# Kernel tuning notes

Hardware: AMD Instinct MI355X
Metric: run time of the kernel (lower is better)

Reference implementation:

```python
import jax, jax.numpy as jnp
import numpy as np

N, C, K, D = 65536, 64, 16, 2
EPS = 1e-5


def batch_norm(x, g, b):
    # training-mode BatchNorm1d over rows (biased variance), x: [rows, C]
    m = x.mean(axis=0)
    v = ((x - m) ** 2).mean(axis=0)
    return (x - m) * jax.lax.rsqrt(v + EPS) * g + b


def setup_inputs() -> dict:
    key = jax.random.key(0)
    ks = jax.random.split(key, 20)
    s = 1.0 / np.sqrt(C)
    inp = {
        "coord": jax.random.normal(ks[0], (N, 3), jnp.float32),
        "feat": jax.random.normal(ks[1], (N, C), jnp.float32),
        "reference_index": jax.random.randint(ks[2], (N, K), 0, N, jnp.int32),
        # per-block stacked params, leading dim D
        "fc1_w": jax.random.uniform(ks[3], (D, C, C), jnp.float32, -s, s),
        "bn1_g": jnp.ones((D, C), jnp.float32),
        "bn1_b": jnp.zeros((D, C), jnp.float32),
        "la_w1": jax.random.uniform(ks[4], (D, C, C), jnp.float32, -s, s),
        "la_b1": jax.random.uniform(ks[5], (D, C), jnp.float32, -s, s),
        "la_bn1_g": jnp.ones((D, C), jnp.float32),
        "la_bn1_b": jnp.zeros((D, C), jnp.float32),
        "la_w2": jax.random.uniform(ks[6], (D, C, C), jnp.float32, -s, s),
        "la_b2": jax.random.uniform(ks[7], (D, C), jnp.float32, -s, s),
        "la_bn2_g": jnp.ones((D, C), jnp.float32),
        "la_bn2_b": jnp.zeros((D, C), jnp.float32),
        "fc3_w": jax.random.uniform(ks[8], (D, C, C), jnp.float32, -s, s),
        "bn2_g": jnp.ones((D, C), jnp.float32),
        "bn2_b": jnp.zeros((D, C), jnp.float32),
        "bn3_g": jnp.ones((D, C), jnp.float32),
        "bn3_b": jnp.zeros((D, C), jnp.float32),
    }
    return inp


def reference(coord, feat, reference_index,
              fc1_w, bn1_g, bn1_b,
              la_w1, la_b1, la_bn1_g, la_bn1_b,
              la_w2, la_b2, la_bn2_g, la_bn2_b,
              fc3_w, bn2_g, bn2_b, bn3_g, bn3_b):
    ref = reference_index  # [n, k]
    for d in range(D):
        identity = feat
        # fc1 (no bias) -> bn1 -> relu
        x = jax.nn.relu(batch_norm(feat @ fc1_w[d].T, bn1_g[d], bn1_b[d]))
        # LocalAggregation: gather neighbors, shared MLP on [n*k, c], max over k
        grouped = x[ref].reshape(-1, C)                      # [n*k, c]
        h = jax.nn.relu(batch_norm(grouped @ la_w1[d].T + la_b1[d],
                                   la_bn1_g[d], la_bn1_b[d]))
        h = jax.nn.relu(batch_norm(h @ la_w2[d].T + la_b2[d],
                                   la_bn2_g[d], la_bn2_b[d]))
        x = h.reshape(ref.shape[0], K, C).max(axis=1)        # [n, c]
        # bn2 -> relu -> fc3 (no bias) -> bn3
        x = jax.nn.relu(batch_norm(x, bn2_g[d], bn2_b[d]))
        x = batch_norm(x @ fc3_w[d].T, bn3_g[d], bn3_b[d])
        feat = jax.nn.relu(identity + x)
    return feat
```

## Files before the change

kernel.cpp:

```cpp
#include <hip/hip_runtime.h>

#define N_PTS 65536
#define BN_EPS 1e-5f
#define NSHD 16
#define NSB  (10 * NSHD * 128)

typedef __attribute__((ext_vector_type(8))) short bf16x8;
typedef __attribute__((ext_vector_type(4))) float f32x4;

static __device__ __forceinline__ unsigned short f2bf(float f) {
    unsigned u = __builtin_bit_cast(unsigned, f);
    u += 0x7fffu + ((u >> 16) & 1u);
    return (unsigned short)(u >> 16);
}
static __device__ __forceinline__ float bf2f(unsigned short h) {
    unsigned u = ((unsigned)h) << 16;
    return __builtin_bit_cast(float, u);
}
static __device__ __forceinline__ unsigned pack2(float a, float b) {
    return (unsigned)f2bf(a) | ((unsigned)f2bf(b) << 16);
}

template<int PRE, int BIAS, int WTD, int OUTBF, int INBF, int HIST>
__global__ __launch_bounds__(256, 4) void mm_kernel(
    const void*  __restrict__ inv_,  const float* __restrict__ identity,
    const float* __restrict__ Wg,    const float* __restrict__ bias,
    const float* __restrict__ gg,    const float* __restrict__ bb,
    const float* __restrict__ S_in,  float inv_denom,
    void*        __restrict__ outv,  float* __restrict__ S_out,
    const unsigned* __restrict__ cw, float* __restrict__ f1_out,
    const int* __restrict__ ref,     unsigned* __restrict__ hdst)
{
    __shared__ unsigned short lwh[64][72], lwl[64][72];
    __shared__ float stg[4][16][68];
    __shared__ float sc[64], sh[64];
    __shared__ float LS[4][64], LQ[4][64];

    const int tid  = threadIdx.x;
    const int lane = tid & 63, wid = tid >> 6;
    const int l15  = lane & 15, kg = lane >> 4;
    const int brow = blockIdx.x * 64;
    const int arow = brow + wid * 16 + l15;

    const int wr = tid >> 2, wc = (tid & 3) * 16;
    const float4* wp = (const float4*)(Wg + wr * 64 + wc);
    float4 wv0 = wp[0], wv1 = wp[1], wv2 = wp[2], wv3 = wp[3];

    float xv[2][8];
    uint4 ub0, ub1;
    float4 a0, a1, a2, a3;
    if (INBF) {
        const uint4* ap = (const uint4*)((const unsigned*)inv_ +
                                         (size_t)arow * 32 + kg * 4);
        ub0 = ap[0]; ub1 = ap[4];
    } else {
        const float4* ap = (const float4*)((const float*)inv_ +
                                           (size_t)arow * 64 + kg * 8);
        a0 = ap[0]; a1 = ap[1]; a2 = ap[8]; a3 = ap[9];
    }
    float4 i0, i1, i2, i3;
    if (PRE == 2) {
        const float4* ip = (const float4*)(identity + (size_t)arow * 64 + kg * 8);
        i0 = ip[0]; i1 = ip[1]; i2 = ip[8]; i3 = ip[9];
    }
    uint4 cc;
    if (WTD) cc = ((const uint4*)(cw + brow + wid * 16))[kg];
    if (HIST) {
        int4 hv = ((const int4*)(ref + brow * 16))[tid];
        atomicAdd(&hdst[hv.x], 1u); atomicAdd(&hdst[hv.y], 1u);
        atomicAdd(&hdst[hv.z], 1u); atomicAdd(&hdst[hv.w], 1u);
    }

    {
        float wf[16] = {wv0.x,wv0.y,wv0.z,wv0.w, wv1.x,wv1.y,wv1.z,wv1.w,
                        wv2.x,wv2.y,wv2.z,wv2.w, wv3.x,wv3.y,wv3.z,wv3.w};
        unsigned ph[8], pl[8];
        #pragma unroll
        for (int q = 0; q < 8; ++q) {
            unsigned short h0 = f2bf(wf[2*q]),   h1 = f2bf(wf[2*q+1]);
            unsigned short l0 = f2bf(wf[2*q]   - bf2f(h0));
            unsigned short l1 = f2bf(wf[2*q+1] - bf2f(h1));
            ph[q] = (unsigned)h0 | ((unsigned)h1 << 16);
            pl[q] = (unsigned)l0 | ((unsigned)l1 << 16);
        }
        uint4* dh = (uint4*)(&lwh[wr][wc]);
        uint4* dl = (uint4*)(&lwl[wr][wc]);
        dh[0] = make_uint4(ph[0], ph[1], ph[2], ph[3]);
        dh[1] = make_uint4(ph[4], ph[5], ph[6], ph[7]);
        dl[0] = make_uint4(pl[0], pl[1], pl[2], pl[3]);
        dl[1] = make_uint4(pl[4], pl[5], pl[6], pl[7]);
    }

    if (PRE >= 1) {
        if (tid < 64) {
            float s = 0.f, q = 0.f;
            #pragma unroll
            for (int g = 0; g < NSHD; ++g) {
                s += S_in[g * 128 + tid];
                q += S_in[g * 128 + 64 + tid];
            }
            float m   = s * inv_denom;
            float var = q * inv_denom - m * m;
            float scl = gg[tid] * rsqrtf(var + BN_EPS);
            sc[tid] = scl; sh[tid] = bb[tid] - m * scl;
        }
    }
    __syncthreads();

    if (INBF) {
        uint4 uu[2] = {ub0, ub1};
        #pragma unroll
        for (int ks = 0; ks < 2; ++ks) {
            unsigned w0 = uu[ks].x, w1 = uu[ks].y, w2 = uu[ks].z, w3 = uu[ks].w;
            xv[ks][0] = bf2f((unsigned short)(w0 & 0xffffu));
            xv[ks][1] = bf2f((unsigned short)(w0 >> 16));
            xv[ks][2] = bf2f((unsigned short)(w1 & 0xffffu));
            xv[ks][3] = bf2f((unsigned short)(w1 >> 16));
            xv[ks][4] = bf2f((unsigned short)(w2 & 0xffffu));
            xv[ks][5] = bf2f((unsigned short)(w2 >> 16));
            xv[ks][6] = bf2f((unsigned short)(w3 & 0xffffu));
            xv[ks][7] = bf2f((unsigned short)(w3 >> 16));
        }
    } else {
        xv[0][0]=a0.x; xv[0][1]=a0.y; xv[0][2]=a0.z; xv[0][3]=a0.w;
        xv[0][4]=a1.x; xv[0][5]=a1.y; xv[0][6]=a1.z; xv[0][7]=a1.w;
        xv[1][0]=a2.x; xv[1][1]=a2.y; xv[1][2]=a2.z; xv[1][3]=a2.w;
        xv[1][4]=a3.x; xv[1][5]=a3.y; xv[1][6]=a3.z; xv[1][7]=a3.w;
    }

    if (PRE == 1) {
        #pragma unroll
        for (int ks = 0; ks < 2; ++ks)
            #pragma unroll
            for (int j = 0; j < 8; ++j) {
                int k = ks * 32 + kg * 8 + j;
                xv[ks][j] = fmaxf(xv[ks][j] * sc[k] + sh[k], 0.f);
            }
    } else if (PRE == 2) {
        float idv[2][8];
        idv[0][0]=i0.x; idv[0][1]=i0.y; idv[0][2]=i0.z; idv[0][3]=i0.w;
        idv[0][4]=i1.x; idv[0][5]=i1.y; idv[0][6]=i1.z; idv[0][7]=i1.w;
        idv[1][0]=i2.x; idv[1][1]=i2.y; idv[1][2]=i2.z; idv[1][3]=i2.w;
        idv[1][4]=i3.x; idv[1][5]=i3.y; idv[1][6]=i3.z; idv[1][7]=i3.w;
        #pragma unroll
        for (int ks = 0; ks < 2; ++ks) {
            #pragma unroll
            for (int j = 0; j < 8; ++j) {
                int k = ks * 32 + kg * 8 + j;
                xv[ks][j] = fmaxf(idv[ks][j] + xv[ks][j] * sc[k] + sh[k], 0.f);
            }
            float* f1p = f1_out + (size_t)arow * 64 + kg * 8 + ks * 32;
            *(float4*)(f1p)     = make_float4(xv[ks][0], xv[ks][1], xv[ks][2], xv[ks][3]);
            *(float4*)(f1p + 4) = make_float4(xv[ks][4], xv[ks][5], xv[ks][6], xv[ks][7]);
        }
    }

    bf16x8 ahi[2], alo[2];
    #pragma unroll
    for (int ks = 0; ks < 2; ++ks) {
        bf16x8 th, tl;
        #pragma unroll
        for (int j = 0; j < 8; ++j) {
            unsigned short h = f2bf(xv[ks][j]);
            th[j] = (short)h;
            tl[j] = (short)f2bf(xv[ks][j] - bf2f(h));
        }
        ahi[ks] = th; alo[ks] = tl;
    }
    f32x4 d[4];
    #pragma unroll
    for (int ct = 0; ct < 4; ++ct) {
        float bc = BIAS ? bias[ct * 16 + l15] : 0.f;
        d[ct] = (f32x4){bc, bc, bc, bc};
    }
    #pragma unroll
    for (int ct = 0; ct < 4; ++ct) {
        const int gcol = ct * 16 + l15;
        #pragma unroll
        for (int ks = 0; ks < 2; ++ks) {
            bf16x8 wh = *(const bf16x8*)(&lwh[gcol][ks * 32 + kg * 8]);
            bf16x8 wl = *(const bf16x8*)(&lwl[gcol][ks * 32 + kg * 8]);
            d[ct] = __builtin_amdgcn_mfma_f32_16x16x32_bf16(ahi[ks], wh, d[ct], 0, 0, 0);
            d[ct] = __builtin_amdgcn_mfma_f32_16x16x32_bf16(alo[ks], wh, d[ct], 0, 0, 0);
            d[ct] = __builtin_amdgcn_mfma_f32_16x16x32_bf16(ahi[ks], wl, d[ct], 0, 0, 0);
        }
    }

    float wt[4] = {1.f, 1.f, 1.f, 1.f};
    if (WTD) {
        wt[0] = (float)cc.x; wt[1] = (float)cc.y;
        wt[2] = (float)cc.z; wt[3] = (float)cc.w;
    }
    float ts[4], tq[4];
    #pragma unroll
    for (int ct = 0; ct < 4; ++ct) {
        float t = 0.f, t2 = 0.f;
        #pragma unroll
        for (int i = 0; i < 4; ++i) {
            float v = d[ct][i];
            t += wt[i] * v; t2 += wt[i] * v * v;
        }
        ts[ct] = t; tq[ct] = t2;
    }

    #pragma unroll
    for (int ct = 0; ct < 4; ++ct)
        #pragma unroll
        for (int i = 0; i < 4; ++i)
            stg[wid][kg * 4 + i][ct * 16 + l15] = d[ct][i];
    __syncthreads();
    if (!OUTBF) {
        float* op = (float*)outv + (size_t)arow * 64 + kg * 16;
        const float* srow = &stg[wid][l15][kg * 16];
        *(float4*)(op + 0)  = *(const float4*)(srow + 0);
        *(float4*)(op + 4)  = *(const float4*)(srow + 4);
        *(float4*)(op + 8)  = *(const float4*)(srow + 8);
        *(float4*)(op + 12) = *(const float4*)(srow + 12);
    } else {
        const float* srow = &stg[wid][l15][kg * 16];
        unsigned pk[8];
        #pragma unroll
        for (int q = 0; q < 8; ++q) pk[q] = pack2(srow[2 * q], srow[2 * q + 1]);
        unsigned* op = (unsigned*)outv;
        uint4* dst = (uint4*)(op + (size_t)arow * 32 + kg * 8);
        dst[0] = make_uint4(pk[0], pk[1], pk[2], pk[3]);
        dst[1] = make_uint4(pk[4], pk[5], pk[6], pk[7]);
    }

    #pragma unroll
    for (int ct = 0; ct < 4; ++ct) {
        float a = ts[ct], b = tq[ct];
        a += __shfl_xor(a, 16);  a += __shfl_xor(a, 32);
        b += __shfl_xor(b, 16);  b += __shfl_xor(b, 32);
        if (kg == 0) { LS[wid][ct * 16 + l15] = a; LQ[wid][ct * 16 + l15] = b; }
    }
    __syncthreads();
    const int bsel = blockIdx.x & (NSHD - 1);
    if (tid < 64)
        atomicAdd(S_out + bsel * 128 + tid,
                  LS[0][tid] + LS[1][tid] + LS[2][tid] + LS[3][tid]);
    else if (tid < 128) {
        int c = tid - 64;
        atomicAdd(S_out + bsel * 128 + 64 + c,
                  LQ[0][c] + LQ[1][c] + LQ[2][c] + LQ[3][c]);
    }
}

__global__ __launch_bounds__(256) void gather_kernel(
    const unsigned* __restrict__ y3u, const int* __restrict__ ref,
    const float* __restrict__ S_in, float inv_denom,
    const float* __restrict__ gg, const float* __restrict__ bb,
    unsigned* __restrict__ xmu, float* __restrict__ S_out)
{
    __shared__ float scs[64], shs[64], Rs[256], Rq[256];
    const int tid = threadIdx.x;
    const int lane = tid & 63, wid = tid >> 6;
    const int c2 = lane & 31;
    const int hsel = lane & 32;
    const int p = blockIdx.x * 4 + wid;
    const int r = 2 * p + (hsel ? 1 : 0);

    int jv = ref[r * 16 + (lane & 15)];
    unsigned u[16];
    #pragma unroll
    for (int t = 0; t < 16; ++t) {
        int j = __shfl(jv, hsel + t);
        u[t] = y3u[(size_t)j * 32 + c2];
    }

    if (tid < 64) {
        float s = 0.f, q = 0.f;
        #pragma unroll
        for (int g = 0; g < NSHD; ++g) {
            s += S_in[g * 128 + tid];
            q += S_in[g * 128 + 64 + tid];
        }
        float m   = s * inv_denom;
        float var = q * inv_denom - m * m;
        float scl = gg[tid] * rsqrtf(var + BN_EPS);
        scs[tid] = scl; shs[tid] = bb[tid] - m * scl;
    }
    __syncthreads();

    float m0 = bf2f((unsigned short)(u[0] & 0xffffu));
    float m1 = bf2f((unsigned short)(u[0] >> 16));
    #pragma unroll
    for (int t = 1; t < 16; ++t) {
        m0 = fmaxf(m0, bf2f((unsigned short)(u[t] & 0xffffu)));
        m1 = fmaxf(m1, bf2f((unsigned short)(u[t] >> 16)));
    }
    float x0 = fmaxf(m0 * scs[2*c2]   + shs[2*c2],   0.f);
    float x1 = fmaxf(m1 * scs[2*c2+1] + shs[2*c2+1], 0.f);
    xmu[(size_t)r * 32 + c2] = pack2(x0, x1);

    const int bsel = blockIdx.x & (NSHD - 1);
    Rs[tid] = x0; Rq[tid] = x0 * x0;
    __syncthreads();
    if (tid < 32) {
        float a = 0.f, c = 0.f;
        #pragma unroll
        for (int i = 0; i < 8; ++i) { a += Rs[tid + 32*i]; c += Rq[tid + 32*i]; }
        atomicAdd(S_out + bsel*128 + 2*tid, a);
        atomicAdd(S_out + bsel*128 + 64 + 2*tid, c);
    }
    __syncthreads();
    Rs[tid] = x1; Rq[tid] = x1 * x1;
    __syncthreads();
    if (tid < 32) {
        float a = 0.f, c = 0.f;
        #pragma unroll
        for (int i = 0; i < 8; ++i) { a += Rs[tid + 32*i]; c += Rq[tid + 32*i]; }
        atomicAdd(S_out + bsel*128 + 2*tid + 1, a);
        atomicAdd(S_out + bsel*128 + 64 + 2*tid + 1, c);
    }
}

__global__ __launch_bounds__(256) void res_final(
    float* __restrict__ io, const float* __restrict__ y4,
    const float* __restrict__ S_in, float inv_denom,
    const float* __restrict__ gg, const float* __restrict__ bb)
{
    __shared__ float sc[64], sh[64];
    const int tid = threadIdx.x;
    int i = blockIdx.x * 256 + tid;
    float4 idv = ((const float4*)io)[i];
    float4 yv  = ((const float4*)y4)[i];
    if (tid < 64) {
        float s = 0.f, q = 0.f;
        #pragma unroll
        for (int g = 0; g < NSHD; ++g) {
            s += S_in[g * 128 + tid];
            q += S_in[g * 128 + 64 + tid];
        }
        float m   = s * inv_denom;
        float var = q * inv_denom - m * m;
        float scl = gg[tid] * rsqrtf(var + BN_EPS);
        sc[tid] = scl; sh[tid] = bb[tid] - m * scl;
    }
    __syncthreads();
    int c0 = (i * 4) & 63;
    float4 o;
    o.x = fmaxf(idv.x + yv.x * sc[c0+0] + sh[c0+0], 0.f);
    o.y = fmaxf(idv.y + yv.y * sc[c0+1] + sh[c0+1], 0.f);
    o.z = fmaxf(idv.z + yv.z * sc[c0+2] + sh[c0+2], 0.f);
    o.w = fmaxf(idv.w + yv.w * sc[c0+3] + sh[c0+3], 0.f);
    ((float4*)io)[i] = o;
}

extern "C" void kernel_launch(void* const* d_in, const int* in_sizes, int n_in,
                              void* d_out, int out_size, void* d_ws, size_t ws_size,
                              hipStream_t stream)
{
    const float* feat    = (const float*)d_in[1];
    const int*   ref     = (const int*)  d_in[2];
    const float* fc1_w   = (const float*)d_in[3];
    const float* bn1_g   = (const float*)d_in[4];
    const float* bn1_b   = (const float*)d_in[5];
    const float* la_w1   = (const float*)d_in[6];
    const float* la_b1   = (const float*)d_in[7];
    const float* la_bn1g = (const float*)d_in[8];
    const float* la_bn1b = (const float*)d_in[9];
    const float* la_w2   = (const float*)d_in[10];
    const float* la_b2   = (const float*)d_in[11];
    const float* la_bn2g = (const float*)d_in[12];
    const float* la_bn2b = (const float*)d_in[13];
    const float* fc3_w   = (const float*)d_in[14];
    const float* bn2_g   = (const float*)d_in[15];
    const float* bn2_b   = (const float*)d_in[16];
    const float* bn3_g   = (const float*)d_in[17];
    const float* bn3_b   = (const float*)d_in[18];
    float* out = (float*)d_out;

    char* base = (char*)d_ws;
    float*    R1  = (float*)base;
    float*    R2  = (float*)(base + 16u * 1024 * 1024);
    unsigned* cnt = (unsigned*)(base + 32u * 1024 * 1024);
    float*    Sb  = (float*)(cnt + N_PTS);
#define SS(i) (Sb + (i) * NSHD * 128)

    hipMemsetAsync(cnt, 0, N_PTS * sizeof(unsigned) + NSB * sizeof(float), stream);

    const float invN  = 1.f / (float)N_PTS;
    const float invNK = invN / 16.f;
    const int MMG = N_PTS / 64;

    mm_kernel<0,0,0,0,0,1><<<MMG,256,0,stream>>>(feat, nullptr, fc1_w,
        nullptr, nullptr, nullptr, nullptr, 0.f, R1, SS(0), nullptr, nullptr, ref, cnt);
    mm_kernel<1,1,1,0,0,0><<<MMG,256,0,stream>>>(R1, nullptr, la_w1,
        la_b1, bn1_g, bn1_b, SS(0), invN, R2, SS(1), cnt, nullptr, nullptr, nullptr);
    mm_kernel<1,1,1,1,0,0><<<MMG,256,0,stream>>>(R2, nullptr, la_w2,
        la_b2, la_bn1g, la_bn1b, SS(1), invNK, R1, SS(2), cnt, nullptr, nullptr, nullptr);
    gather_kernel<<<8192,256,0,stream>>>((const unsigned*)R1, ref, SS(2), invNK,
        la_bn2g, la_bn2b, (unsigned*)R2, SS(3));
    mm_kernel<1,0,0,0,1,0><<<MMG,256,0,stream>>>(R2, nullptr, fc3_w,
        nullptr, bn2_g, bn2_b, SS(3), invN, R1, SS(4), nullptr, nullptr, nullptr, nullptr);

    mm_kernel<2,0,0,0,0,0><<<MMG,256,0,stream>>>(R1, feat, fc1_w + 4096,
        nullptr, bn3_g, bn3_b, SS(4), invN, R2, SS(5), nullptr, out, nullptr, nullptr);
    mm_kernel<1,1,1,0,0,0><<<MMG,256,0,stream>>>(R2, nullptr, la_w1 + 4096,
        la_b1 + 64, bn1_g + 64, bn1_b + 64, SS(5), invN, R1, SS(6), cnt, nullptr, nullptr, nullptr);
    mm_kernel<1,1,1,1,0,0><<<MMG,256,0,stream>>>(R1, nullptr, la_w2 + 4096,
        la_b2 + 64, la_bn1g + 64, la_bn1b + 64, SS(6), invNK, R2, SS(7), cnt, nullptr, nullptr, nullptr);
    gather_kernel<<<8192,256,0,stream>>>((const unsigned*)R2, ref, SS(7), invNK,
        la_bn2g + 64, la_bn2b + 64, (unsigned*)R1, SS(8));
    mm_kernel<1,0,0,0,1,0><<<MMG,256,0,stream>>>(R1, nullptr, fc3_w + 4096,
        nullptr, bn2_g + 64, bn2_b + 64, SS(8), invN, R2, SS(9), nullptr, nullptr, nullptr, nullptr);
    res_final<<<(N_PTS * 64 / 4) / 256, 256, 0, stream>>>(out, R2, SS(9), invN,
        bn3_g + 64, bn3_b + 64);
}
```

Before: 221.4 us.

## Widen BN stat shards, parallelize shard reduction, and double gather work per block

Raises the number of atomic statistic shards from 16 to 64 to reduce atomic contention. Each consumer kernel now reduces those shards with all 256 threads, two halves combined in shared memory, instead of 64 threads looping serially. The gather kernel handles two point pairs per wave, halving the grid and the number of atomics. The cost is a larger memset, more shard reads per block and extra barriers.

```diff
diff --git a/kernel.cpp b/kernel.cpp
--- a/kernel.cpp
+++ b/kernel.cpp
@@ -2,7 +2,7 @@
 
 #define N_PTS 65536
 #define BN_EPS 1e-5f
-#define NSHD 16
+#define NSHD 64
 #define NSB  (10 * NSHD * 128)
 
 typedef __attribute__((ext_vector_type(8))) short bf16x8;
@@ -35,6 +35,7 @@
     __shared__ float stg[4][16][68];
     __shared__ float sc[64], sh[64];
     __shared__ float LS[4][64], LQ[4][64];
+    float* PS = &stg[0][0][0];
 
     const int tid  = threadIdx.x;
     const int lane = tid & 63, wid = tid >> 6;
@@ -92,13 +93,17 @@
     }
 
     if (PRE >= 1) {
+        const int idx = tid & 127, hh = tid >> 7;
+        float acc = 0.f;
+        #pragma unroll
+        for (int g = 0; g < NSHD / 2; ++g)
+            acc += S_in[(hh * (NSHD / 2) + g) * 128 + idx];
+        PS[hh * 128 + idx] = acc;
+        __syncthreads();
+        if (tid < 128) PS[tid] += PS[128 + tid];
+        __syncthreads();
         if (tid < 64) {
-            float s = 0.f, q = 0.f;
-            #pragma unroll
-            for (int g = 0; g < NSHD; ++g) {
-                s += S_in[g * 128 + tid];
-                q += S_in[g * 128 + 64 + tid];
-            }
+            float s = PS[tid], q = PS[64 + tid];
             float m   = s * inv_denom;
             float var = q * inv_denom - m * m;
             float scl = gg[tid] * rsqrtf(var + BN_EPS);
@@ -252,49 +257,71 @@
     const float* __restrict__ gg, const float* __restrict__ bb,
     unsigned* __restrict__ xmu, float* __restrict__ S_out)
 {
-    __shared__ float scs[64], shs[64], Rs[256], Rq[256];
+    __shared__ float scs[64], shs[64], Rs[256], Rq[256], PS[256];
     const int tid = threadIdx.x;
     const int lane = tid & 63, wid = tid >> 6;
     const int c2 = lane & 31;
     const int hsel = lane & 32;
-    const int p = blockIdx.x * 4 + wid;
-    const int r = 2 * p + (hsel ? 1 : 0);
-
-    int jv = ref[r * 16 + (lane & 15)];
-    unsigned u[16];
+    const int p0 = blockIdx.x * 8 + wid * 2;
+    const int r0 = 2 * p0 + (hsel ? 1 : 0);
+    const int r1 = r0 + 2;
+
+    int jv0 = ref[r0 * 16 + (lane & 15)];
+    int jv1 = ref[r1 * 16 + (lane & 15)];
+    unsigned u0[16], u1[16];
     #pragma unroll
     for (int t = 0; t < 16; ++t) {
-        int j = __shfl(jv, hsel + t);
-        u[t] = y3u[(size_t)j * 32 + c2];
-    }
-
-    if (tid < 64) {
-        float s = 0.f, q = 0.f;
-        #pragma unroll
-        for (int g = 0; g < NSHD; ++g) {
-            s += S_in[g * 128 + tid];
-            q += S_in[g * 128 + 64 + tid];
-        }
-        float m   = s * inv_denom;
-        float var = q * inv_denom - m * m;
-        float scl = gg[tid] * rsqrtf(var + BN_EPS);
-        scs[tid] = scl; shs[tid] = bb[tid] - m * scl;
-    }
-    __syncthreads();
-
-    float m0 = bf2f((unsigned short)(u[0] & 0xffffu));
-    float m1 = bf2f((unsigned short)(u[0] >> 16));
-    #pragma unroll
-    for (int t = 1; t < 16; ++t) {
-        m0 = fmaxf(m0, bf2f((unsigned short)(u[t] & 0xffffu)));
-        m1 = fmaxf(m1, bf2f((unsigned short)(u[t] >> 16)));
-    }
-    float x0 = fmaxf(m0 * scs[2*c2]   + shs[2*c2],   0.f);
-    float x1 = fmaxf(m1 * scs[2*c2+1] + shs[2*c2+1], 0.f);
-    xmu[(size_t)r * 32 + c2] = pack2(x0, x1);
+        int j = __shfl(jv0, hsel + t);
+        u0[t] = y3u[(size_t)j * 32 + c2];
+    }
+    #pragma unroll
+    for (int t = 0; t < 16; ++t) {
+        int j = __shfl(jv1, hsel + t);
+        u1[t] = y3u[(size_t)j * 32 + c2];
+    }
+
+    {
+        const int idx = tid & 127, hh = tid >> 7;
+        float acc = 0.f;
+        #pragma unroll
+        for (int g = 0; g < NSHD / 2; ++g)
+            acc += S_in[(hh * (NSHD / 2) + g) * 128 + idx];
+        PS[hh * 128 + idx] = acc;
+        __syncthreads();
+        if (tid < 128) PS[tid] += PS[128 + tid];
+        __syncthreads();
+        if (tid < 64) {
+            float s = PS[tid], q = PS[64 + tid];
+            float m   = s * inv_denom;
+            float var = q * inv_denom - m * m;
+            float scl = gg[tid] * rsqrtf(var + BN_EPS);
+            scs[tid] = scl; shs[tid] = bb[tid] - m * scl;
+        }
+        __syncthreads();
+    }
+    const float sc0 = scs[2*c2], sc1 = scs[2*c2+1];
+    const float sh0 = shs[2*c2], sh1 = shs[2*c2+1];
+
+    float s0 = 0.f, q0 = 0.f, s1 = 0.f, q1 = 0.f;
+    #pragma unroll
+    for (int pair = 0; pair < 2; ++pair) {
+        const unsigned* u = pair ? u1 : u0;
+        const int r = pair ? r1 : r0;
+        float m0 = bf2f((unsigned short)(u[0] & 0xffffu));
+        float m1 = bf2f((unsigned short)(u[0] >> 16));
+        #pragma unroll
+        for (int t = 1; t < 16; ++t) {
+            m0 = fmaxf(m0, bf2f((unsigned short)(u[t] & 0xffffu)));
+            m1 = fmaxf(m1, bf2f((unsigned short)(u[t] >> 16)));
+        }
+        float x0 = fmaxf(m0 * sc0 + sh0, 0.f);
+        float x1 = fmaxf(m1 * sc1 + sh1, 0.f);
+        xmu[(size_t)r * 32 + c2] = pack2(x0, x1);
+        s0 += x0; q0 += x0 * x0; s1 += x1; q1 += x1 * x1;
+    }
 
     const int bsel = blockIdx.x & (NSHD - 1);
-    Rs[tid] = x0; Rq[tid] = x0 * x0;
+    Rs[tid] = s0; Rq[tid] = q0;
     __syncthreads();
     if (tid < 32) {
         float a = 0.f, c = 0.f;
@@ -304,7 +331,7 @@
         atomicAdd(S_out + bsel*128 + 64 + 2*tid, c);
     }
     __syncthreads();
-    Rs[tid] = x1; Rq[tid] = x1 * x1;
+    Rs[tid] = s1; Rq[tid] = q1;
     __syncthreads();
     if (tid < 32) {
         float a = 0.f, c = 0.f;
@@ -320,24 +347,30 @@
     const float* __restrict__ S_in, float inv_denom,
     const float* __restrict__ gg, const float* __restrict__ bb)
 {
-    __shared__ float sc[64], sh[64];
+    __shared__ float sc[64], sh[64], PS[256];
     const int tid = threadIdx.x;
     int i = blockIdx.x * 256 + tid;
     float4 idv = ((const float4*)io)[i];
     float4 yv  = ((const float4*)y4)[i];
-    if (tid < 64) {
-        float s = 0.f, q = 0.f;
-        #pragma unroll
-        for (int g = 0; g < NSHD; ++g) {
-            s += S_in[g * 128 + tid];
-            q += S_in[g * 128 + 64 + tid];
-        }
-        float m   = s * inv_denom;
-        float var = q * inv_denom - m * m;
-        float scl = gg[tid] * rsqrtf(var + BN_EPS);
-        sc[tid] = scl; sh[tid] = bb[tid] - m * scl;
-    }
-    __syncthreads();
+    {
+        const int idx = tid & 127, hh = tid >> 7;
+        float acc = 0.f;
+        #pragma unroll
+        for (int g = 0; g < NSHD / 2; ++g)
+            acc += S_in[(hh * (NSHD / 2) + g) * 128 + idx];
+        PS[hh * 128 + idx] = acc;
+        __syncthreads();
+        if (tid < 128) PS[tid] += PS[128 + tid];
+        __syncthreads();
+        if (tid < 64) {
+            float s = PS[tid], q = PS[64 + tid];
+            float m   = s * inv_denom;
+            float var = q * inv_denom - m * m;
+            float scl = gg[tid] * rsqrtf(var + BN_EPS);
+            sc[tid] = scl; sh[tid] = bb[tid] - m * scl;
+        }
+        __syncthreads();
+    }
     int c0 = (i * 4) & 63;
     float4 o;
     o.x = fmaxf(idv.x + yv.x * sc[c0+0] + sh[c0+0], 0.f);
@@ -390,7 +423,7 @@
         la_b1, bn1_g, bn1_b, SS(0), invN, R2, SS(1), cnt, nullptr, nullptr, nullptr);
     mm_kernel<1,1,1,1,0,0><<<MMG,256,0,stream>>>(R2, nullptr, la_w2,
         la_b2, la_bn1g, la_bn1b, SS(1), invNK, R1, SS(2), cnt, nullptr, nullptr, nullptr);
-    gather_kernel<<<8192,256,0,stream>>>((const unsigned*)R1, ref, SS(2), invNK,
+    gather_kernel<<<4096,256,0,stream>>>((const unsigned*)R1, ref, SS(2), invNK,
         la_bn2g, la_bn2b, (unsigned*)R2, SS(3));
     mm_kernel<1,0,0,0,1,0><<<MMG,256,0,stream>>>(R2, nullptr, fc3_w,
         nullptr, bn2_g, bn2_b, SS(3), invN, R1, SS(4), nullptr, nullptr, nullptr, nullptr);
@@ -401,7 +434,7 @@
         la_b1 + 64, bn1_g + 64, bn1_b + 64, SS(5), invN, R1, SS(6), cnt, nullptr, nullptr, nullptr);
     mm_kernel<1,1,1,1,0,0><<<MMG,256,0,stream>>>(R1, nullptr, la_w2 + 4096,
         la_b2 + 64, la_bn1g + 64, la_bn1b + 64, SS(6), invNK, R2, SS(7), cnt, nullptr, nullptr, nullptr);
-    gather_kernel<<<8192,256,0,stream>>>((const unsigned*)R2, ref, SS(7), invNK,
+    gather_kernel<<<4096,256,0,stream>>>((const unsigned*)R2, ref, SS(7), invNK,
         la_bn2g + 64, la_bn2b + 64, (unsigned*)R1, SS(8));
     mm_kernel<1,0,0,0,1,0><<<MMG,256,0,stream>>>(R1, nullptr, fc3_w + 4096,
         nullptr, bn2_g + 64, bn2_b + 64, SS(8), invN, R2, SS(9), nullptr, nullptr, nullptr, nullptr);
```

After: 203.8 us. -8.0%, faster.
